# Performance work log

Hardware: AMD Instinct MI355X
Metric: run time of the kernel (lower is better)

Reference implementation:

```python
import jax, jax.numpy as jnp
import numpy as np

# TT ranks: source list [1,7,7,7,1] interpreted as r_0..r_4 with wraparound r_5 = r_0 = 1
RANKS = [1, 7, 7, 7, 1, 1]
LAYERS = [
    ([7, 4, 4, 4, 7], [8, 8, 8, 8, 4]),   # 3136 -> 16384
    ([8, 8, 8, 8, 4], [8, 8, 8, 4, 4]),   # 16384 -> 8192
    ([8, 8, 8, 4, 4], [8, 8, 4, 4, 4]),   # 8192 -> 4096
    ([8, 8, 4, 4, 4], [8, 4, 4, 4, 4]),   # 4096 -> 2048
    ([8, 4, 4, 4, 4], [10, 1, 1, 1, 1]),  # 2048 -> 10 (out_modes padded with 1s)
]
BATCH = 8192


def tt_linear(x, cores, bias):
    # x: [B, in_features]; cores[i]: [r_i, m_i, n_i, r_{i+1}]
    B = x.shape[0]
    t = x.reshape(B, -1, 1, 1)  # [B, M_remaining, N_done, r]
    for G in cores:
        r0, m, n, r1 = G.shape
        rest = t.shape[1] // m
        t = t.reshape(B, m, rest, t.shape[2], r0)
        # contract current input mode m and incoming rank r0 with the core
        t = jnp.einsum('bmsnp,pmoq->bsnoq', t, G)  # [B, rest, N_done, n, r1]
        t = t.reshape(B, rest, -1, r1)
    return t.reshape(B, -1) + bias  # [B, out_features]


def setup_inputs() -> dict:
    key = jax.random.key(0)
    keys = jax.random.split(key, 32)
    inp = {"x": jax.random.normal(keys[0], (BATCH, 3136), jnp.float32)}
    ki = 1
    for li, (im, om) in enumerate(LAYERS, start=1):
        for ci in range(5):
            shape = (RANKS[ci], im[ci], om[ci], RANKS[ci + 1])
            scale = 1.0 / np.sqrt(im[ci] * RANKS[ci])
            inp[f"l{li}_core{ci}"] = jax.random.normal(keys[ki], shape, jnp.float32) * scale
            ki += 1
        inp[f"l{li}_bias"] = jnp.zeros((int(np.prod(om)),), jnp.float32)
    return inp


def reference(x,
              l1_core0, l1_core1, l1_core2, l1_core3, l1_core4, l1_bias,
              l2_core0, l2_core1, l2_core2, l2_core3, l2_core4, l2_bias,
              l3_core0, l3_core1, l3_core2, l3_core3, l3_core4, l3_bias,
              l4_core0, l4_core1, l4_core2, l4_core3, l4_core4, l4_bias,
              l5_core0, l5_core1, l5_core2, l5_core3, l5_core4, l5_bias):
    h = jax.nn.relu(tt_linear(x, [l1_core0, l1_core1, l1_core2, l1_core3, l1_core4], l1_bias))
    h = jax.nn.relu(tt_linear(h, [l2_core0, l2_core1, l2_core2, l2_core3, l2_core4], l2_bias))
    h = jax.nn.relu(tt_linear(h, [l3_core0, l3_core1, l3_core2, l3_core3, l3_core4], l3_bias))
    h = jax.nn.relu(tt_linear(h, [l4_core0, l4_core1, l4_core2, l4_core3, l4_core4], l4_bias))
    logits = tt_linear(h, [l5_core0, l5_core1, l5_core2, l5_core3, l5_core4], l5_bias)
    return jax.nn.softmax(logits, axis=1)
```

## Files before the change

kernel.cpp:

```cpp
#include <hip/hip_runtime.h>
#include <stdint.h>
#include <stddef.h>

typedef _Float16 f16;
typedef _Float16 f16x8 __attribute__((ext_vector_type(8)));
typedef float    f32x4 __attribute__((ext_vector_type(4)));

#define NB 8192

struct Ptrs {
  const float *G0[5], *G1[5], *G2[5], *G3[5], *bias[5];
  float *T01[5], *T23[5], *biasr[5];
  f16   *WHt[5];
};

__global__ void prep1_kernel(Ptrs p) {
  constexpr int IM[5][5] = {{7,4,4,4,7},{8,8,8,8,4},{8,8,8,4,4},{8,8,4,4,4},{8,4,4,4,4}};
  constexpr int OM[5][5] = {{8,8,8,8,4},{8,8,8,4,4},{8,8,4,4,4},{8,4,4,4,4},{10,1,1,1,1}};
  const int job = blockIdx.x;
  const int tid = threadIdx.x;
  if (job < 5) {
    const int L = job;
    const int m1=IM[L][1], n0=OM[L][0], n1=OM[L][1];
    const int n01 = n0*n1;
    const int cnt = IM[L][0]*m1*n01*7;
    const float* G0 = p.G0[L]; const float* G1 = p.G1[L];
    float* T = p.T01[L];
    for (int e = tid; e < cnt; e += blockDim.x) {
      const int r2  = e % 7;
      const int j01 = (e/7) % n01;
      const int i01 = e / (7*n01);
      const int i0 = i01/m1, i1 = i01 - i0*m1;
      const int j0 = j01/n1, j1 = j01 - j0*n1;
      float s = 0.f;
      for (int r1 = 0; r1 < 7; ++r1)
        s += G0[(i0*n0 + j0)*7 + r1] * G1[((r1*m1 + i1)*n1 + j1)*7 + r2];
      T[e] = s;
    }
  } else if (job < 10) {
    const int L = job - 5;
    const int m2=IM[L][2], m3=IM[L][3], n2=OM[L][2], n3=OM[L][3];
    const int n23 = n2*n3;
    const int cnt = m2*m3*n23*7;
    const float* G2 = p.G2[L]; const float* G3 = p.G3[L];
    float* T = p.T23[L];
    for (int e = tid; e < cnt; e += blockDim.x) {
      const int r2  = e % 7;
      const int j23 = (e/7) % n23;
      const int i23 = e / (7*n23);
      const int i2 = i23/m3, i3 = i23 - i2*m3;
      const int j2 = j23/n3, j3 = j23 - j2*n3;
      float s = 0.f;
      for (int r3 = 0; r3 < 7; ++r3)
        s += G2[((r2*m2 + i2)*n2 + j2)*7 + r3] * G3[(r3*m3 + i3)*n3 + j3];
      T[e] = s;
    }
  } else {
    const int L = job - 10;
    constexpr int OUTF[5] = {16384, 8192, 4096, 2048, 10};
    constexpr int N4[5]   = {4,4,4,4,1};
    const int of = OUTF[L], n4 = N4[L], outH = of / n4;
    const float* b = p.bias[L];
    float* br = p.biasr[L];
    for (int e = tid; e < of; e += blockDim.x) {
      const int j4 = e / outH, jH = e - j4*outH;
      br[e] = b[jH*n4 + j4];
    }
  }
}

__global__ void prep2_kernel(Ptrs p) {
  constexpr int INH[5]  = {448, 4096, 2048, 1024, 512};
  constexpr int M23[5]  = {16, 64, 32, 16, 16};
  constexpr int N23[5]  = {64, 32, 16, 16, 1};
  constexpr int N01[5]  = {64, 64, 64, 32, 10};
  constexpr int BASE[6] = {0, 1835008, 10223616, 12320768, 12845056, 12850176};
  const int total = BASE[5];
  for (int e = blockIdx.x*blockDim.x + threadIdx.x; e < total;
       e += gridDim.x*blockDim.x) {
    int L = 0;
    while (L < 4 && e >= BASE[L+1]) ++L;
    const int le = e - BASE[L];
    const int iH = le % INH[L];
    const int jH = le / INH[L];
    const int i01 = iH / M23[L], i23 = iH - i01*M23[L];
    const int j01 = jH / N23[L], j23 = jH - j01*N23[L];
    const float* a = p.T01[L] + (i01*N01[L] + j01)*7;
    const float* b = p.T23[L] + (i23*N23[L] + j23)*7;
    float s = 0.f;
#pragma unroll
    for (int r = 0; r < 7; ++r) s += a[r]*b[r];
    p.WHt[L][le] = (f16)s;
  }
}

__global__ void stagea_x(const float* __restrict__ x, const float* __restrict__ g4,
                         f16* __restrict__ u, int BC) {
  const int idx = blockIdx.x*blockDim.x + threadIdx.x;
  if (idx >= BC*448) return;
  const int b = idx / 448, c = idx - b*448;
  const float* xr = x + (size_t)b*3136 + c*7;
  float v[7];
#pragma unroll
  for (int i = 0; i < 7; ++i) v[i] = xr[i];
#pragma unroll
  for (int j = 0; j < 4; ++j) {
    float s = 0.f;
#pragma unroll
    for (int i = 0; i < 7; ++i) s += v[i]*g4[i*4+j];
    u[(size_t)(b*4+j)*448 + c] = (f16)s;
  }
}

__global__ void __launch_bounds__(256, 2)
gemm_fused(const f16* __restrict__ A, const f16* __restrict__ Bt,
           f16* __restrict__ U, const float* __restrict__ biasr,
           const float* __restrict__ g4n,
           int N, int K, int n4n)
{
  __shared__ f16 Ls[2][2][128*64];

  const int tid  = threadIdx.x;
  const int wid  = tid >> 6, lane = tid & 63;
  const int wr   = wid >> 1, wc = wid & 1;
  const int l15  = lane & 15, l4 = lane >> 4, lm = l15 & 7;

  const int nwg = gridDim.x;
  int wg = blockIdx.x;
  if ((nwg & 7) == 0) wg = (wg & 7) * (nwg >> 3) + (wg >> 3);
  const int Nt = N >> 7;
  const int bx = wg / Nt, by = wg - bx * Nt;
  const int m0 = bx << 7, n0 = by << 7;

  const int rr   = tid >> 3;
  const int cs8  = (((tid & 7) ^ (rr & 7)) << 3);
  const int dst0 = wid << 9;

  int axoff[2], bxoff[2];
#pragma unroll
  for (int h = 0; h < 2; ++h) {
    const int cz = (((h << 2) + l4) ^ lm) << 3;
    axoff[h] = ((wr << 6) + l15) * 64 + cz;
    bxoff[h] = ((wc << 6) + l15) * 64 + cz;
  }

  f32x4 acc[4][4] = {};

  auto stage = [&](int buf, int kt) {
    const f16* gA = A + (size_t)m0 * K + kt;
    const f16* gB = Bt + (size_t)n0 * K + kt;
    f16* dA = &Ls[buf][0][0];
    f16* dB = &Ls[buf][1][0];
#pragma unroll
    for (int q = 0; q < 4; ++q)
      __builtin_amdgcn_global_load_lds(
          (const __attribute__((address_space(1))) void*)(gA + (size_t)(q*32 + rr)*K + cs8),
          (__attribute__((address_space(3))) void*)(dA + q*2048 + dst0), 16, 0, 0);
#pragma unroll
    for (int q = 0; q < 4; ++q)
      __builtin_amdgcn_global_load_lds(
          (const __attribute__((address_space(1))) void*)(gB + (size_t)(q*32 + rr)*K + cs8),
          (__attribute__((address_space(3))) void*)(dB + q*2048 + dst0), 16, 0, 0);
  };

  stage(0, 0);
  __syncthreads();
  const int nt = K >> 6;
  int cur = 0;
  for (int t = 0; t < nt; ++t) {
    if (t + 1 < nt) stage(cur ^ 1, (t + 1) << 6);
    __builtin_amdgcn_sched_barrier(0);
    const f16* As = &Ls[cur][0][0];
    const f16* Bs = &Ls[cur][1][0];
#pragma unroll
    for (int h = 0; h < 2; ++h) {
      f16x8 af[4], bf[4];
#pragma unroll
      for (int n = 0; n < 4; ++n) bf[n] = *(const f16x8*)(Bs + bxoff[h] + n*1024);
#pragma unroll
      for (int m = 0; m < 4; ++m) af[m] = *(const f16x8*)(As + axoff[h] + m*1024);
      __builtin_amdgcn_s_setprio(1);
#pragma unroll
      for (int m = 0; m < 4; ++m)
#pragma unroll
        for (int n = 0; n < 4; ++n)
          acc[m][n] = __builtin_amdgcn_mfma_f32_16x16x32_f16(af[m], bf[n], acc[m][n], 0, 0, 0);
      __builtin_amdgcn_s_setprio(0);
    }
    __syncthreads();
    cur ^= 1;
  }

#pragma unroll
  for (int m = 0; m < 4; ++m) {
    const int rb = m0 + (wr << 6) + (m << 4) + (l4 << 2);
    const int b  = rb >> 2;
#pragma unroll
    for (int n = 0; n < 4; ++n) {
      const int col = n0 + (wc << 6) + (n << 4) + l15;
      float v[4];
#pragma unroll
      for (int r = 0; r < 4; ++r)
        v[r] = fmaxf(acc[m][n][r] + biasr[(size_t)r * N + col], 0.f);
      if (n4n == 4) {
#pragma unroll
        for (int j = 0; j < 4; ++j) {
          float s = v[0]*g4n[j] + v[1]*g4n[4+j] + v[2]*g4n[8+j] + v[3]*g4n[12+j];
          U[(size_t)(b*4 + j) * N + col] = (f16)s;
        }
      } else {
        float s = v[0]*g4n[0] + v[1]*g4n[1] + v[2]*g4n[2] + v[3]*g4n[3];
        U[(size_t)b * N + col] = (f16)s;
      }
    }
  }
}

__global__ void l5_softmax(const f16* __restrict__ u, const f16* __restrict__ Wt,
                           const float* __restrict__ bias, float* __restrict__ out)
{
  const int wid = threadIdx.x >> 6, lane = threadIdx.x & 63;
  const int row = blockIdx.x*4 + wid;
  float acc[10] = {};
  const f16* ur = u + (size_t)row*512;
#pragma unroll
  for (int t = 0; t < 8; ++t) {
    const float a = (float)ur[t*64 + lane];
#pragma unroll
    for (int j = 0; j < 10; ++j)
      acc[j] += a * (float)Wt[j*512 + t*64 + lane];
  }
#pragma unroll
  for (int j = 0; j < 10; ++j) {
#pragma unroll
    for (int s = 32; s; s >>= 1) acc[j] += __shfl_xor(acc[j], s);
    acc[j] += bias[j];
  }
  float mx = acc[0];
#pragma unroll
  for (int j = 1; j < 10; ++j) mx = fmaxf(mx, acc[j]);
  float sum = 0.f;
#pragma unroll
  for (int j = 0; j < 10; ++j) { acc[j] = __expf(acc[j]-mx); sum += acc[j]; }
  const float inv = 1.f / sum;
  if (lane < 10) out[(size_t)row*10 + lane] = acc[lane]*inv;
}

extern "C" void kernel_launch(void* const* d_in, const int* in_sizes, int n_in,
                              void* d_out, int out_size, void* d_ws, size_t ws_size,
                              hipStream_t stream) {
  (void)in_sizes; (void)n_in; (void)out_size;
  const float* x = (const float*)d_in[0];
  Ptrs p;
  const float* G4[5];
  for (int L = 0; L < 5; ++L) {
    p.G0[L]   = (const float*)d_in[1 + L*6 + 0];
    p.G1[L]   = (const float*)d_in[1 + L*6 + 1];
    p.G2[L]   = (const float*)d_in[1 + L*6 + 2];
    p.G3[L]   = (const float*)d_in[1 + L*6 + 3];
    G4[L]     = (const float*)d_in[1 + L*6 + 4];
    p.bias[L] = (const float*)d_in[1 + L*6 + 5];
  }

  uintptr_t w = (uintptr_t)d_ws;
  auto alloc = [&](size_t bytes) {
    uintptr_t r = w; w += (bytes + 255) & ~(size_t)255; return (void*)r;
  };
  constexpr int  t01sz[5] = {12544, 28672, 28672, 14336, 2240};
  constexpr int  t23sz[5] = {7168, 14336, 3584, 1792, 112};
  constexpr int  brsz[5]  = {16384, 8192, 4096, 2048, 10};
  constexpr long whsz[5]  = {448L*4096, 4096L*2048, 2048L*1024, 1024L*512, 512L*10};
  for (int L = 0; L < 5; ++L) p.T01[L]   = (float*)alloc((size_t)t01sz[L]*4);
  for (int L = 0; L < 5; ++L) p.T23[L]   = (float*)alloc((size_t)t23sz[L]*4);
  for (int L = 0; L < 5; ++L) p.biasr[L] = (float*)alloc((size_t)brsz[L]*4);
  for (int L = 0; L < 5; ++L) p.WHt[L]   = (f16*)alloc((size_t)whsz[L]*2);
  const size_t fixedBytes = (size_t)(w - (uintptr_t)d_ws);

  int BC = 0;
  for (int c = NB; c >= 32; c >>= 1)
    if (fixedBytes + (size_t)c * (16384 + 32768) <= ws_size) { BC = c; break; }
  if (!BC) return;
  f16* bufA = (f16*)alloc((size_t)BC*16384);
  f16* bufB = (f16*)alloc((size_t)BC*32768);

  prep1_kernel<<<15, 256, 0, stream>>>(p);
  prep2_kernel<<<4096, 256, 0, stream>>>(p);

  const int nch = NB / BC;
  const int Mt = (BC*4)/128;
  for (int ch = 0; ch < nch; ++ch) {
    const size_t cs = (size_t)ch * BC;
    stagea_x<<<(BC*448 + 255)/256, 256, 0, stream>>>(x + cs*3136, G4[0], bufA, BC);
    gemm_fused<<<Mt*32, 256, 0, stream>>>(bufA, p.WHt[0], bufB, p.biasr[0],
                                          G4[1], 4096, 448, 4);
    gemm_fused<<<Mt*16, 256, 0, stream>>>(bufB, p.WHt[1], bufA, p.biasr[1],
                                          G4[2], 2048, 4096, 4);
    gemm_fused<<<Mt*8, 256, 0, stream>>>(bufA, p.WHt[2], bufB, p.biasr[2],
                                         G4[3], 1024, 2048, 4);
    gemm_fused<<<Mt*4, 256, 0, stream>>>(bufB, p.WHt[3], bufA, p.biasr[3],
                                         G4[4], 512, 1024, 1);
    l5_softmax<<<BC/4, 256, 0, stream>>>(bufA, p.WHt[4], p.biasr[4],
                                         (float*)d_out + cs*10);
  }
}
```

Baseline: 1.087 ms.

## Add 256x256-tile GEMM kernel with 8 waves for the first three layers

```diff
diff --git a/kernel.cpp b/kernel.cpp
--- a/kernel.cpp
+++ b/kernel.cpp
@@ -112,6 +112,110 @@
   }
 }
 
+__global__ void __launch_bounds__(512, 2)
+gemm256(const f16* __restrict__ A, const f16* __restrict__ Bt,
+        f16* __restrict__ U, const float* __restrict__ biasr,
+        const float* __restrict__ g4n,
+        int N, int K, int n4n)
+{
+  __shared__ f16 Ls[2][2][256*64];
+
+  const int tid  = threadIdx.x;
+  const int wid  = tid >> 6, lane = tid & 63;
+  const int wr   = wid >> 2, wc = wid & 3;
+  const int l15  = lane & 15, l4 = lane >> 4, lm = l15 & 7;
+
+  const int nwg = gridDim.x;
+  int wg = blockIdx.x;
+  if ((nwg & 7) == 0) wg = (wg & 7) * (nwg >> 3) + (wg >> 3);
+  const int Nt = N >> 8;
+  const int bx = wg / Nt, by = wg - bx * Nt;
+  const int m0 = bx << 8, n0 = by << 8;
+
+  const int rr   = tid >> 3;
+  const int cs8  = (((tid & 7) ^ (rr & 7)) << 3);
+  const int dst0 = tid << 3;
+
+  int axoff[2], bxoff[2];
+#pragma unroll
+  for (int h = 0; h < 2; ++h) {
+    const int cz = (((h << 2) + l4) ^ lm) << 3;
+    axoff[h] = ((wr << 7) + l15) * 64 + cz;
+    bxoff[h] = ((wc << 6) + l15) * 64 + cz;
+  }
+
+  f32x4 acc[8][4] = {};
+
+  auto stage = [&](int buf, int kt) {
+    const f16* gA = A + (size_t)m0 * K + kt;
+    const f16* gB = Bt + (size_t)n0 * K + kt;
+    f16* dA = &Ls[buf][0][0];
+    f16* dB = &Ls[buf][1][0];
+#pragma unroll
+    for (int q = 0; q < 4; ++q)
+      __builtin_amdgcn_global_load_lds(
+          (const __attribute__((address_space(1))) void*)(gA + (size_t)(q*64 + rr)*K + cs8),
+          (__attribute__((address_space(3))) void*)(dA + q*4096 + dst0), 16, 0, 0);
+#pragma unroll
+    for (int q = 0; q < 4; ++q)
+      __builtin_amdgcn_global_load_lds(
+          (const __attribute__((address_space(1))) void*)(gB + (size_t)(q*64 + rr)*K + cs8),
+          (__attribute__((address_space(3))) void*)(dB + q*4096 + dst0), 16, 0, 0);
+  };
+
+  stage(0, 0);
+  __syncthreads();
+  const int nt = K >> 6;
+  int cur = 0;
+  for (int t = 0; t < nt; ++t) {
+    if (t + 1 < nt) stage(cur ^ 1, (t + 1) << 6);
+    __builtin_amdgcn_sched_barrier(0);
+    const f16* As = &Ls[cur][0][0];
+    const f16* Bs = &Ls[cur][1][0];
+#pragma unroll
+    for (int h = 0; h < 2; ++h) {
+      f16x8 af[8], bf[4];
+#pragma unroll
+      for (int n = 0; n < 4; ++n) bf[n] = *(const f16x8*)(Bs + bxoff[h] + n*1024);
+#pragma unroll
+      for (int m = 0; m < 8; ++m) af[m] = *(const f16x8*)(As + axoff[h] + m*1024);
+      __builtin_amdgcn_s_setprio(1);
+#pragma unroll
+      for (int m = 0; m < 8; ++m)
+#pragma unroll
+        for (int n = 0; n < 4; ++n)
+          acc[m][n] = __builtin_amdgcn_mfma_f32_16x16x32_f16(af[m], bf[n], acc[m][n], 0, 0, 0);
+      __builtin_amdgcn_s_setprio(0);
+    }
+    __syncthreads();
+    cur ^= 1;
+  }
+
+#pragma unroll
+  for (int m = 0; m < 8; ++m) {
+    const int rb = m0 + (wr << 7) + (m << 4) + (l4 << 2);
+    const int b  = rb >> 2;
+#pragma unroll
+    for (int n = 0; n < 4; ++n) {
+      const int col = n0 + (wc << 6) + (n << 4) + l15;
+      float v[4];
+#pragma unroll
+      for (int r = 0; r < 4; ++r)
+        v[r] = fmaxf(acc[m][n][r] + biasr[(size_t)r * N + col], 0.f);
+      if (n4n == 4) {
+#pragma unroll
+        for (int j = 0; j < 4; ++j) {
+          float s = v[0]*g4n[j] + v[1]*g4n[4+j] + v[2]*g4n[8+j] + v[3]*g4n[12+j];
+          U[(size_t)(b*4 + j) * N + col] = (f16)s;
+        }
+      } else {
+        float s = v[0]*g4n[0] + v[1]*g4n[1] + v[2]*g4n[2] + v[3]*g4n[3];
+        U[(size_t)b * N + col] = (f16)s;
+      }
+    }
+  }
+}
+
 __global__ void __launch_bounds__(256, 2)
 gemm_fused(const f16* __restrict__ A, const f16* __restrict__ Bt,
            f16* __restrict__ U, const float* __restrict__ biasr,
@@ -277,7 +381,7 @@
   const size_t fixedBytes = (size_t)(w - (uintptr_t)d_ws);
 
   int BC = 0;
-  for (int c = NB; c >= 32; c >>= 1)
+  for (int c = NB; c >= 64; c >>= 1)
     if (fixedBytes + (size_t)c * (16384 + 32768) <= ws_size) { BC = c; break; }
   if (!BC) return;
   f16* bufA = (f16*)alloc((size_t)BC*16384);
@@ -287,18 +391,18 @@
   prep2_kernel<<<4096, 256, 0, stream>>>(p);
 
   const int nch = NB / BC;
-  const int Mt = (BC*4)/128;
+  const int M   = BC * 4;
   for (int ch = 0; ch < nch; ++ch) {
     const size_t cs = (size_t)ch * BC;
     stagea_x<<<(BC*448 + 255)/256, 256, 0, stream>>>(x + cs*3136, G4[0], bufA, BC);
-    gemm_fused<<<Mt*32, 256, 0, stream>>>(bufA, p.WHt[0], bufB, p.biasr[0],
-                                          G4[1], 4096, 448, 4);
-    gemm_fused<<<Mt*16, 256, 0, stream>>>(bufB, p.WHt[1], bufA, p.biasr[1],
-                                          G4[2], 2048, 4096, 4);
-    gemm_fused<<<Mt*8, 256, 0, stream>>>(bufA, p.WHt[2], bufB, p.biasr[2],
-                                         G4[3], 1024, 2048, 4);
-    gemm_fused<<<Mt*4, 256, 0, stream>>>(bufB, p.WHt[3], bufA, p.biasr[3],
-                                         G4[4], 512, 1024, 1);
+    gemm256<<<(M/256)*(4096/256), 512, 0, stream>>>(bufA, p.WHt[0], bufB, p.biasr[0],
+                                                    G4[1], 4096, 448, 4);
+    gemm256<<<(M/256)*(2048/256), 512, 0, stream>>>(bufB, p.WHt[1], bufA, p.biasr[1],
+                                                    G4[2], 2048, 4096, 4);
+    gemm256<<<(M/256)*(1024/256), 512, 0, stream>>>(bufA, p.WHt[2], bufB, p.biasr[2],
+                                                    G4[3], 1024, 2048, 4);
+    gemm_fused<<<(M/128)*(512/128), 256, 0, stream>>>(bufB, p.WHt[3], bufA, p.biasr[3],
+                                                      G4[4], 512, 1024, 1);
     l5_softmax<<<BC/4, 256, 0, stream>>>(bufA, p.WHt[4], p.biasr[4],
                                          (float*)d_out + cs*10);
   }
```

Measured after the change: 970.1 us. 1.12x faster.
